# Optimization experiments

Measured on AMD Instinct MI355X. Metric: run time of the kernel, lower is better.

The kernel has to match this reference:

```python
import jax, jax.numpy as jnp
import numpy as np

LN_EPS = 1e-5  # torch.nn.LayerNorm default eps


def setup_inputs() -> dict:
    key = jax.random.key(0)
    k1, k2 = jax.random.split(key)
    x = jax.random.normal(k1, (16384, 2048), dtype=jnp.float32)
    # torch Linear weight layout: [out_features, in_features]
    W = jax.random.normal(k2, (2048, 2048), dtype=jnp.float32) * (1.0 / np.sqrt(2048))
    return {"x": x, "W": W}


def reference(x, W):
    # LayerNorm over last dim, elementwise_affine=False
    mean = jnp.mean(x, axis=-1, keepdims=True)
    var = jnp.mean(jnp.square(x - mean), axis=-1, keepdims=True)
    xn = (x - mean) * jax.lax.rsqrt(var + LN_EPS)
    # Linear (no bias): y = xn @ W.T, then sigmoid
    y = jnp.einsum("td,od->to", xn, W)
    return jax.nn.sigmoid(y)
```

## Files before the change

kernel.cpp:

```cpp
#include <hip/hip_runtime.h>
#include <hip/hip_bf16.h>
#include <stdint.h>


typedef __attribute__((ext_vector_type(4))) float f32x4;
typedef __attribute__((ext_vector_type(8))) __bf16 b16x8;

__device__ __forceinline__ void async16(void* lds, const void* g) {
  __builtin_amdgcn_global_load_lds(
      (const __attribute__((address_space(1))) void*)g,
      (__attribute__((address_space(3))) void*)lds, 16, 0, 0);
}

__device__ __forceinline__ unsigned short f2bf(float f) {
  uint32_t u = __float_as_uint(f);
  u += 0x7FFFu + ((u >> 16) & 1u);
  return (unsigned short)(u >> 16);
}

__global__ __launch_bounds__(256) void ln_bf16_kernel(
    const float* __restrict__ x, unsigned short* __restrict__ xn) {
  const int row = blockIdx.x;
  const int t = threadIdx.x;
  const float4* xr = (const float4*)(x + (size_t)row * 2048);
  float4 a = xr[t];
  float4 b = xr[t + 256];
  float s = a.x + a.y + a.z + a.w + b.x + b.y + b.z + b.w;
  float q = a.x * a.x + a.y * a.y + a.z * a.z + a.w * a.w +
            b.x * b.x + b.y * b.y + b.z * b.z + b.w * b.w;
#pragma unroll
  for (int off = 32; off > 0; off >>= 1) {
    s += __shfl_down(s, off);
    q += __shfl_down(q, off);
  }
  __shared__ float red[8];
  const int w = t >> 6;
  if ((t & 63) == 0) { red[w] = s; red[4 + w] = q; }
  __syncthreads();
  s = red[0] + red[1] + red[2] + red[3];
  q = red[4] + red[5] + red[6] + red[7];
  const float mean = s * (1.0f / 2048.0f);
  const float var = fmaxf(q * (1.0f / 2048.0f) - mean * mean, 0.0f);
  const float scl = rsqrtf(var + 1e-5f);
  ushort4 o0, o1;
  o0.x = f2bf((a.x - mean) * scl);
  o0.y = f2bf((a.y - mean) * scl);
  o0.z = f2bf((a.z - mean) * scl);
  o0.w = f2bf((a.w - mean) * scl);
  o1.x = f2bf((b.x - mean) * scl);
  o1.y = f2bf((b.y - mean) * scl);
  o1.z = f2bf((b.z - mean) * scl);
  o1.w = f2bf((b.w - mean) * scl);
  ushort4* orow = (ushort4*)(xn + (size_t)row * 2048);
  orow[t] = o0;
  orow[t + 256] = o1;
}

__global__ __launch_bounds__(256) void wconv_kernel(
    const float* __restrict__ W, unsigned short* __restrict__ Wb) {
  const size_t i = (size_t)blockIdx.x * 256 + threadIdx.x;
  float4 v = ((const float4*)W)[i];
  ushort4 o;
  o.x = f2bf(v.x);
  o.y = f2bf(v.y);
  o.z = f2bf(v.z);
  o.w = f2bf(v.w);
  ((ushort4*)Wb)[i] = o;
}


#define STG_A(buf, h, kt)                                              \
  do {                                                                 \
    const char* s_ = pA + (size_t)((h) * 128) * 4096 + (kt) * 128;     \
    char* d_ = lds + (buf) * 65536 + (h) * 16384 + tid * 16;           \
    async16(d_, s_);                                                   \
    async16(d_ + 8192, s_ + 64 * 4096);                                \
  } while (0)

#define STG_B(buf, h, kt)                                              \
  do {                                                                 \
    const char* s_ = pB + (size_t)((h) * 128) * 4096 + (kt) * 128;     \
    char* d_ = lds + 32768 + (buf) * 65536 + (h) * 16384 + tid * 16;   \
    async16(d_, s_);                                                   \
    async16(d_ + 8192, s_ + 64 * 4096);                                \
  } while (0)

#define LDA(buf, qm)                                                   \
  do {                                                                 \
    _Pragma("unroll") for (int i_ = 0; i_ < 4; ++i_) {                 \
      const char* p_ = lds + (buf) * 65536 + (qm) * 16384 + abase + i_ * 2048; \
      aF[i_][0] = *(const b16x8*)(p_ + cs0);                           \
      aF[i_][1] = *(const b16x8*)(p_ + cs1);                           \
    }                                                                  \
  } while (0)

#define LDB(dstf, buf, qn)                                             \
  do {                                                                 \
    _Pragma("unroll") for (int j_ = 0; j_ < 2; ++j_) {                 \
      const char* p_ = lds + (buf) * 65536 + (qn) * 16384 + bbase + j_ * 2048; \
      dstf[j_][0] = *(const b16x8*)(p_ + cs0);                         \
      dstf[j_][1] = *(const b16x8*)(p_ + cs1);                         \
    }                                                                  \
  } while (0)

#define MFMA_Q(qm, qn, BF)                                             \
  do {                                                                 \
    __builtin_amdgcn_s_setprio(1);                                     \
    _Pragma("unroll") for (int i_ = 0; i_ < 4; ++i_) {                 \
      _Pragma("unroll") for (int j_ = 0; j_ < 2; ++j_) {               \
        f32x4 c_ = acc[(qm) * 4 + i_][(qn) * 2 + j_];                  \
        c_ = __builtin_amdgcn_mfma_f32_16x16x32_bf16(aF[i_][0], BF[j_][0], c_, 0, 0, 0); \
        c_ = __builtin_amdgcn_mfma_f32_16x16x32_bf16(aF[i_][1], BF[j_][1], c_, 0, 0, 0); \
        acc[(qm) * 4 + i_][(qn) * 2 + j_] = c_;                        \
      }                                                                \
    }                                                                  \
    __builtin_amdgcn_s_setprio(0);                                     \
  } while (0)

#define BAR1                                                           \
  do {                                                                 \
    __builtin_amdgcn_s_barrier();                                      \
    asm volatile("s_waitcnt lgkmcnt(0)" ::: "memory");                 \
    __builtin_amdgcn_sched_barrier(0);                                 \
  } while (0)

#define BAR2                                                           \
  do {                                                                 \
    __builtin_amdgcn_s_barrier();                                      \
    asm volatile("" ::: "memory");                                     \
  } while (0)

#define VMC(n) asm volatile("s_waitcnt vmcnt(" #n ")" ::: "memory")

__global__ __launch_bounds__(512, 2) void gemm8p(
    const unsigned short* __restrict__ A, const unsigned short* __restrict__ B,
    float* __restrict__ C) {
  __shared__ __align__(16) char lds[131072];

  const int bid0 = blockIdx.x;
  const int bid = (bid0 & 7) * 64 + (bid0 >> 3);
  const int bm = bid >> 3;
  const int bn = bid & 7;

  const int tid = threadIdx.x;
  const int w = tid >> 6, l = tid & 63;
  const int wr = w >> 2, wc = w & 3;
  const int fr = l & 15, fg = l >> 4;

  const int arow = tid >> 3;
  const int swz = ((tid & 7) << 4) ^ ((arow & 7) << 4);
  const char* pA = (const char*)A + (size_t)(bm * 256 + arow) * 4096 + swz;
  const char* pB = (const char*)B + (size_t)(bn * 256 + arow) * 4096 + swz;

  const int cswz = (fg << 4) ^ ((fr & 7) << 4);
  const int cs0 = cswz, cs1 = cswz ^ 64;
  const int abase = (wr * 64 + fr) * 128;
  const int bbase = 32768 + (wc * 32 + fr) * 128;

  f32x4 acc[8][4] = {};
  b16x8 aF[4][2], b0F[2][2], b1F[2][2];

  STG_A(0, 0, 0); STG_B(0, 0, 0); STG_B(0, 1, 0); STG_A(0, 1, 0);
  STG_B(1, 0, 1); STG_A(1, 0, 1); STG_B(1, 1, 1);
  VMC(6);
  __builtin_amdgcn_s_barrier();
  asm volatile("" ::: "memory");

#pragma unroll 1
  for (int it = 0; it < 16; ++it) {
    const int t1 = 2 * it + 1, t2 = 2 * it + 2, t3 = 2 * it + 3;
    const bool s2 = (t2 < 32), s3 = (t3 < 32);

    LDA(0, 0); LDB(b0F, 0, 0);
    STG_A(1, 1, t1);
    BAR1; MFMA_Q(0, 0, b0F); BAR2;

    LDB(b1F, 0, 1);
    if (s2) STG_B(0, 0, t2);
    BAR1; MFMA_Q(0, 1, b1F); BAR2;

    LDA(0, 1);
    if (s2) STG_A(0, 0, t2);
    BAR1; MFMA_Q(1, 1, b1F); BAR2;

    if (s2) STG_B(0, 1, t2);
    BAR1; MFMA_Q(1, 0, b0F);
    if (it < 15) { VMC(6); } else { VMC(0); }
    BAR2;

    LDA(1, 0); LDB(b0F, 1, 0);
    if (s2) STG_A(0, 1, t2);
    BAR1; MFMA_Q(0, 0, b0F); BAR2;

    LDB(b1F, 1, 1);
    if (s3) STG_B(1, 0, t3);
    BAR1; MFMA_Q(0, 1, b1F); BAR2;

    LDA(1, 1);
    if (s3) STG_A(1, 0, t3);
    BAR1; MFMA_Q(1, 1, b1F); BAR2;

    if (s3) STG_B(1, 1, t3);
    BAR1; MFMA_Q(1, 0, b0F);
    if (it < 15) { VMC(6); }
    BAR2;
  }

  float* gC = C + (size_t)(bm * 256) * 2048 + bn * 256;
#pragma unroll
  for (int qm = 0; qm < 2; ++qm) {
#pragma unroll
    for (int i = 0; i < 4; ++i) {
#pragma unroll
      for (int qn = 0; qn < 2; ++qn) {
#pragma unroll
        for (int j = 0; j < 2; ++j) {
#pragma unroll
          for (int r = 0; r < 4; ++r) {
            const int row = qm * 128 + wr * 64 + i * 16 + fg * 4 + r;
            const int col = qn * 128 + wc * 32 + j * 16 + fr;
            const float y = acc[qm * 4 + i][qn * 2 + j][r];
            gC[(size_t)row * 2048 + col] = 1.0f / (1.0f + __expf(-y));
          }
        }
      }
    }
  }
}

extern "C" void kernel_launch(void* const* d_in, const int* in_sizes, int n_in,
                              void* d_out, int out_size, void* d_ws, size_t ws_size,
                              hipStream_t stream) {
  const float* x = (const float*)d_in[0];
  const float* W = (const float*)d_in[1];
  float* out = (float*)d_out;

  unsigned short* xnb = (unsigned short*)d_ws;
  unsigned short* Wb =
      (unsigned short*)((char*)d_ws + (size_t)16384 * 2048 * 2);

  ln_bf16_kernel<<<16384, 256, 0, stream>>>(x, xnb);
  wconv_kernel<<<(2048 * 2048 / 4) / 256, 256, 0, stream>>>(W, Wb);
  gemm8p<<<512, 512, 0, stream>>>(xnb, Wb, out);
}
```

Baseline: 169.9 us.

## Switch GEMM to 32x32x16 MFMA, halve barriers, fuse LN and weight conversion

The GEMM inner tiles move from 16x16x32 to 32x32x16 bf16 MFMA, with the LDS fragment loads and the epilogue row mapping rewritten to match. The two barriers per quarter step become one barrier followed by an LDS wait, and the staging order is shuffled. LayerNorm and the fp32-to-bf16 conversion of W now run in one launch that uses extra blocks, saving a kernel launch. The larger MFMA cuts instruction count and fragment loads per FLOP, but dropping the second barrier relies on the remaining ordering to protect buffer reuse.

Result: slower. 180.4 us (+6.2%).

```diff
diff --git a/kernel.cpp b/kernel.cpp
--- a/kernel.cpp
+++ b/kernel.cpp
@@ -4,12 +4,13 @@
 
 
 typedef __attribute__((ext_vector_type(4))) float f32x4;
+typedef __attribute__((ext_vector_type(16))) float f32x16;
 typedef __attribute__((ext_vector_type(8))) __bf16 b16x8;
 
-__device__ __forceinline__ void async16(void* lds, const void* g) {
+__device__ __forceinline__ void async16(void* lds_p, const void* g) {
   __builtin_amdgcn_global_load_lds(
       (const __attribute__((address_space(1))) void*)g,
-      (__attribute__((address_space(3))) void*)lds, 16, 0, 0);
+      (__attribute__((address_space(3))) void*)lds_p, 16, 0, 0);
 }
 
 __device__ __forceinline__ unsigned short f2bf(float f) {
@@ -18,10 +19,19 @@
   return (unsigned short)(u >> 16);
 }
 
-__global__ __launch_bounds__(256) void ln_bf16_kernel(
-    const float* __restrict__ x, unsigned short* __restrict__ xn) {
+__global__ __launch_bounds__(256) void ln_wconv_kernel(
+    const float* __restrict__ x, unsigned short* __restrict__ xn,
+    const float* __restrict__ W, unsigned short* __restrict__ Wb) {
+  const int t = threadIdx.x;
+  if (blockIdx.x >= 16384) {
+    const size_t i = (size_t)(blockIdx.x - 16384) * 256 + t;
+    float4 v = ((const float4*)W)[i];
+    ushort4 o;
+    o.x = f2bf(v.x); o.y = f2bf(v.y); o.z = f2bf(v.z); o.w = f2bf(v.w);
+    ((ushort4*)Wb)[i] = o;
+    return;
+  }
   const int row = blockIdx.x;
-  const int t = threadIdx.x;
   const float4* xr = (const float4*)(x + (size_t)row * 2048);
   float4 a = xr[t];
   float4 b = xr[t + 256];
@@ -56,18 +66,6 @@
   orow[t + 256] = o1;
 }
 
-__global__ __launch_bounds__(256) void wconv_kernel(
-    const float* __restrict__ W, unsigned short* __restrict__ Wb) {
-  const size_t i = (size_t)blockIdx.x * 256 + threadIdx.x;
-  float4 v = ((const float4*)W)[i];
-  ushort4 o;
-  o.x = f2bf(v.x);
-  o.y = f2bf(v.y);
-  o.z = f2bf(v.z);
-  o.w = f2bf(v.w);
-  ((ushort4*)Wb)[i] = o;
-}
-
 
 #define STG_A(buf, h, kt)                                              \
   do {                                                                 \
@@ -87,47 +85,44 @@
 
 #define LDA(buf, qm)                                                   \
   do {                                                                 \
-    _Pragma("unroll") for (int i_ = 0; i_ < 4; ++i_) {                 \
-      const char* p_ = lds + (buf) * 65536 + (qm) * 16384 + abase + i_ * 2048; \
-      aF[i_][0] = *(const b16x8*)(p_ + cs0);                           \
-      aF[i_][1] = *(const b16x8*)(p_ + cs1);                           \
+    const char* base_ = lds + (buf) * 65536 + (qm) * 16384 + rowA;     \
+    _Pragma("unroll") for (int mi_ = 0; mi_ < 2; ++mi_) {              \
+      _Pragma("unroll") for (int s_ = 0; s_ < 4; ++s_) {               \
+        aF[mi_][s_] = *(const b16x8*)(base_ + mi_ * 4096 + ofs[s_]);   \
+      }                                                                \
     }                                                                  \
   } while (0)
 
 #define LDB(dstf, buf, qn)                                             \
   do {                                                                 \
-    _Pragma("unroll") for (int j_ = 0; j_ < 2; ++j_) {                 \
-      const char* p_ = lds + (buf) * 65536 + (qn) * 16384 + bbase + j_ * 2048; \
-      dstf[j_][0] = *(const b16x8*)(p_ + cs0);                         \
-      dstf[j_][1] = *(const b16x8*)(p_ + cs1);                         \
+    const char* base_ = lds + (buf) * 65536 + 32768 + (qn) * 16384 + rowB; \
+    _Pragma("unroll") for (int s_ = 0; s_ < 4; ++s_) {                 \
+      dstf[s_] = *(const b16x8*)(base_ + ofs[s_]);                     \
     }                                                                  \
   } while (0)
 
 #define MFMA_Q(qm, qn, BF)                                             \
   do {                                                                 \
     __builtin_amdgcn_s_setprio(1);                                     \
-    _Pragma("unroll") for (int i_ = 0; i_ < 4; ++i_) {                 \
-      _Pragma("unroll") for (int j_ = 0; j_ < 2; ++j_) {               \
-        f32x4 c_ = acc[(qm) * 4 + i_][(qn) * 2 + j_];                  \
-        c_ = __builtin_amdgcn_mfma_f32_16x16x32_bf16(aF[i_][0], BF[j_][0], c_, 0, 0, 0); \
-        c_ = __builtin_amdgcn_mfma_f32_16x16x32_bf16(aF[i_][1], BF[j_][1], c_, 0, 0, 0); \
-        acc[(qm) * 4 + i_][(qn) * 2 + j_] = c_;                        \
+    _Pragma("unroll") for (int s_ = 0; s_ < 4; ++s_) {                 \
+      _Pragma("unroll") for (int mi_ = 0; mi_ < 2; ++mi_) {            \
+        acc[(qm) * 2 + mi_][qn] = __builtin_amdgcn_mfma_f32_32x32x16_bf16( \
+            aF[mi_][s_], BF[s_], acc[(qm) * 2 + mi_][qn], 0, 0, 0);    \
       }                                                                \
     }                                                                  \
     __builtin_amdgcn_s_setprio(0);                                     \
   } while (0)
 
-#define BAR1                                                           \
+#define BARR                                                           \
   do {                                                                 \
     __builtin_amdgcn_s_barrier();                                      \
+    asm volatile("" ::: "memory");                                     \
+  } while (0)
+
+#define LGKM0                                                          \
+  do {                                                                 \
     asm volatile("s_waitcnt lgkmcnt(0)" ::: "memory");                 \
     __builtin_amdgcn_sched_barrier(0);                                 \
-  } while (0)
-
-#define BAR2                                                           \
-  do {                                                                 \
-    __builtin_amdgcn_s_barrier();                                      \
-    asm volatile("" ::: "memory");                                     \
   } while (0)
 
 #define VMC(n) asm volatile("s_waitcnt vmcnt(" #n ")" ::: "memory")
@@ -145,83 +140,81 @@
   const int tid = threadIdx.x;
   const int w = tid >> 6, l = tid & 63;
   const int wr = w >> 2, wc = w & 3;
-  const int fr = l & 15, fg = l >> 4;
+  const int l31 = l & 31;
+  const int h16 = (l >> 5) * 16;
+  const int sw7 = (l & 7) << 4;
 
   const int arow = tid >> 3;
   const int swz = ((tid & 7) << 4) ^ ((arow & 7) << 4);
   const char* pA = (const char*)A + (size_t)(bm * 256 + arow) * 4096 + swz;
   const char* pB = (const char*)B + (size_t)(bn * 256 + arow) * 4096 + swz;
 
-  const int cswz = (fg << 4) ^ ((fr & 7) << 4);
-  const int cs0 = cswz, cs1 = cswz ^ 64;
-  const int abase = (wr * 64 + fr) * 128;
-  const int bbase = 32768 + (wc * 32 + fr) * 128;
-
-  f32x4 acc[8][4] = {};
-  b16x8 aF[4][2], b0F[2][2], b1F[2][2];
+  int ofs[4];
+#pragma unroll
+  for (int s = 0; s < 4; ++s) ofs[s] = (s * 32 + h16) ^ sw7;
+  const int rowA = (wr * 64 + l31) * 128;
+  const int rowB = (wc * 32 + l31) * 128;
+
+  f32x16 acc[4][2] = {};
+  b16x8 aF[2][4], bF0[4], bF1[4];
 
   STG_A(0, 0, 0); STG_B(0, 0, 0); STG_B(0, 1, 0); STG_A(0, 1, 0);
   STG_B(1, 0, 1); STG_A(1, 0, 1); STG_B(1, 1, 1);
   VMC(6);
-  __builtin_amdgcn_s_barrier();
-  asm volatile("" ::: "memory");
+  BARR;
 
 #pragma unroll 1
   for (int it = 0; it < 16; ++it) {
     const int t1 = 2 * it + 1, t2 = 2 * it + 2, t3 = 2 * it + 3;
-    const bool s2 = (t2 < 32), s3 = (t3 < 32);
-
-    LDA(0, 0); LDB(b0F, 0, 0);
+    const bool s2 = (it < 15);
+
     STG_A(1, 1, t1);
-    BAR1; MFMA_Q(0, 0, b0F); BAR2;
-
-    LDB(b1F, 0, 1);
-    if (s2) STG_B(0, 0, t2);
-    BAR1; MFMA_Q(0, 1, b1F); BAR2;
-
+    LDA(0, 0); LDB(bF0, 0, 0);
+    BARR; LGKM0; MFMA_Q(0, 0, bF0);
+
+    LDB(bF1, 0, 1);
+    BARR; LGKM0; MFMA_Q(0, 1, bF1);
+
+    if (s2) { STG_B(0, 0, t2); STG_A(0, 0, t2); }
     LDA(0, 1);
-    if (s2) STG_A(0, 0, t2);
-    BAR1; MFMA_Q(1, 1, b1F); BAR2;
+    BARR; LGKM0; MFMA_Q(1, 1, bF1);
 
     if (s2) STG_B(0, 1, t2);
-    BAR1; MFMA_Q(1, 0, b0F);
-    if (it < 15) { VMC(6); } else { VMC(0); }
-    BAR2;
-
-    LDA(1, 0); LDB(b0F, 1, 0);
+    BARR; MFMA_Q(1, 0, bF0);
+    if (s2) { VMC(6); } else { VMC(0); }
+
     if (s2) STG_A(0, 1, t2);
-    BAR1; MFMA_Q(0, 0, b0F); BAR2;
-
-    LDB(b1F, 1, 1);
-    if (s3) STG_B(1, 0, t3);
-    BAR1; MFMA_Q(0, 1, b1F); BAR2;
-
+    LDA(1, 0); LDB(bF0, 1, 0);
+    BARR; LGKM0; MFMA_Q(0, 0, bF0);
+
+    LDB(bF1, 1, 1);
+    BARR; LGKM0; MFMA_Q(0, 1, bF1);
+
+    if (s2) { STG_B(1, 0, t3); STG_A(1, 0, t3); }
     LDA(1, 1);
-    if (s3) STG_A(1, 0, t3);
-    BAR1; MFMA_Q(1, 1, b1F); BAR2;
-
-    if (s3) STG_B(1, 1, t3);
-    BAR1; MFMA_Q(1, 0, b0F);
-    if (it < 15) { VMC(6); }
-    BAR2;
+    BARR; LGKM0; MFMA_Q(1, 1, bF1);
+
+    if (s2) STG_B(1, 1, t3);
+    BARR; MFMA_Q(1, 0, bF0);
+    if (s2) VMC(6);
   }
 
   float* gC = C + (size_t)(bm * 256) * 2048 + bn * 256;
+  const int rbase = 4 * (l >> 5);
 #pragma unroll
   for (int qm = 0; qm < 2; ++qm) {
 #pragma unroll
-    for (int i = 0; i < 4; ++i) {
+    for (int mi = 0; mi < 2; ++mi) {
 #pragma unroll
       for (int qn = 0; qn < 2; ++qn) {
-#pragma unroll
-        for (int j = 0; j < 2; ++j) {
-#pragma unroll
-          for (int r = 0; r < 4; ++r) {
-            const int row = qm * 128 + wr * 64 + i * 16 + fg * 4 + r;
-            const int col = qn * 128 + wc * 32 + j * 16 + fr;
-            const float y = acc[qm * 4 + i][qn * 2 + j][r];
-            gC[(size_t)row * 2048 + col] = 1.0f / (1.0f + __expf(-y));
-          }
+        const f32x16 v = acc[qm * 2 + mi][qn];
+        const int col = qn * 128 + wc * 32 + l31;
+        const int row0 = qm * 128 + wr * 64 + mi * 32 + rbase;
+#pragma unroll
+        for (int r = 0; r < 16; ++r) {
+          const int row = row0 + (r & 3) + 8 * (r >> 2);
+          const float y = v[r];
+          gC[(size_t)row * 2048 + col] = 1.0f / (1.0f + __expf(-y));
         }
       }
     }
@@ -239,7 +232,6 @@
   unsigned short* Wb =
       (unsigned short*)((char*)d_ws + (size_t)16384 * 2048 * 2);
 
-  ln_bf16_kernel<<<16384, 256, 0, stream>>>(x, xnb);
-  wconv_kernel<<<(2048 * 2048 / 4) / 256, 256, 0, stream>>>(W, Wb);
+  ln_wconv_kernel<<<16384 + 4096, 256, 0, stream>>>(x, xnb, W, Wb);
   gemm8p<<<512, 512, 0, stream>>>(xnb, Wb, out);
 }
```

## Software-pipeline LDS fragment loads under MFMAs, fuse LN and weight convert

Applied to the files above, without the earlier changes.

Restructures the GEMM main loop so LDS fragment reads for the next quadrant are issued during the current MFMA batch, splitting MFMA and A-fragment loads into K-halves that interleave. This removes the stalls where waves wait on lgkmcnt before each MFMA group. It also merges the LayerNorm and weight bf16-conversion kernels into one launch and uses a hardware reciprocal in the sigmoid epilogue. The reworked barrier/waitcnt placement raises the risk of LDS race hazards and adds register pressure.

Result: faster. 164.6 us (-3.1%).

```diff
diff --git a/kernel.cpp b/kernel.cpp
--- a/kernel.cpp
+++ b/kernel.cpp
@@ -6,10 +6,10 @@
 typedef __attribute__((ext_vector_type(4))) float f32x4;
 typedef __attribute__((ext_vector_type(8))) __bf16 b16x8;
 
-__device__ __forceinline__ void async16(void* lds, const void* g) {
+__device__ __forceinline__ void async16(void* lds_p, const void* g) {
   __builtin_amdgcn_global_load_lds(
       (const __attribute__((address_space(1))) void*)g,
-      (__attribute__((address_space(3))) void*)lds, 16, 0, 0);
+      (__attribute__((address_space(3))) void*)lds_p, 16, 0, 0);
 }
 
 __device__ __forceinline__ unsigned short f2bf(float f) {
@@ -18,10 +18,19 @@
   return (unsigned short)(u >> 16);
 }
 
-__global__ __launch_bounds__(256) void ln_bf16_kernel(
-    const float* __restrict__ x, unsigned short* __restrict__ xn) {
+__global__ __launch_bounds__(256) void ln_wconv_kernel(
+    const float* __restrict__ x, unsigned short* __restrict__ xn,
+    const float* __restrict__ W, unsigned short* __restrict__ Wb) {
+  const int t = threadIdx.x;
+  if (blockIdx.x >= 16384) {
+    const size_t i = (size_t)(blockIdx.x - 16384) * 256 + t;
+    float4 v = ((const float4*)W)[i];
+    ushort4 o;
+    o.x = f2bf(v.x); o.y = f2bf(v.y); o.z = f2bf(v.z); o.w = f2bf(v.w);
+    ((ushort4*)Wb)[i] = o;
+    return;
+  }
   const int row = blockIdx.x;
-  const int t = threadIdx.x;
   const float4* xr = (const float4*)(x + (size_t)row * 2048);
   float4 a = xr[t];
   float4 b = xr[t + 256];
@@ -56,18 +65,6 @@
   orow[t + 256] = o1;
 }
 
-__global__ __launch_bounds__(256) void wconv_kernel(
-    const float* __restrict__ W, unsigned short* __restrict__ Wb) {
-  const size_t i = (size_t)blockIdx.x * 256 + threadIdx.x;
-  float4 v = ((const float4*)W)[i];
-  ushort4 o;
-  o.x = f2bf(v.x);
-  o.y = f2bf(v.y);
-  o.z = f2bf(v.z);
-  o.w = f2bf(v.w);
-  ((ushort4*)Wb)[i] = o;
-}
-
 
 #define STG_A(buf, h, kt)                                              \
   do {                                                                 \
@@ -85,14 +82,15 @@
     async16(d_ + 8192, s_ + 64 * 4096);                                \
   } while (0)
 
-#define LDA(buf, qm)                                                   \
+#define LDA_S(buf, qm, S)                                              \
   do {                                                                 \
     _Pragma("unroll") for (int i_ = 0; i_ < 4; ++i_) {                 \
       const char* p_ = lds + (buf) * 65536 + (qm) * 16384 + abase + i_ * 2048; \
-      aF[i_][0] = *(const b16x8*)(p_ + cs0);                           \
-      aF[i_][1] = *(const b16x8*)(p_ + cs1);                           \
+      aF[i_][S] = *(const b16x8*)(p_ + ((S) ? cs1 : cs0));             \
     }                                                                  \
   } while (0)
+
+#define LDA(buf, qm) do { LDA_S(buf, qm, 0); LDA_S(buf, qm, 1); } while (0)
 
 #define LDB(dstf, buf, qn)                                             \
   do {                                                                 \
@@ -103,33 +101,35 @@
     }                                                                  \
   } while (0)
 
-#define MFMA_Q(qm, qn, BF)                                             \
+#define MFMA_H(qm, qn, BF, S)                                          \
   do {                                                                 \
     __builtin_amdgcn_s_setprio(1);                                     \
     _Pragma("unroll") for (int i_ = 0; i_ < 4; ++i_) {                 \
       _Pragma("unroll") for (int j_ = 0; j_ < 2; ++j_) {               \
-        f32x4 c_ = acc[(qm) * 4 + i_][(qn) * 2 + j_];                  \
-        c_ = __builtin_amdgcn_mfma_f32_16x16x32_bf16(aF[i_][0], BF[j_][0], c_, 0, 0, 0); \
-        c_ = __builtin_amdgcn_mfma_f32_16x16x32_bf16(aF[i_][1], BF[j_][1], c_, 0, 0, 0); \
-        acc[(qm) * 4 + i_][(qn) * 2 + j_] = c_;                        \
+        acc[(qm) * 4 + i_][(qn) * 2 + j_] =                            \
+            __builtin_amdgcn_mfma_f32_16x16x32_bf16(                   \
+                aF[i_][S], BF[j_][S], acc[(qm) * 4 + i_][(qn) * 2 + j_], 0, 0, 0); \
       }                                                                \
     }                                                                  \
     __builtin_amdgcn_s_setprio(0);                                     \
   } while (0)
 
-#define BAR1                                                           \
+#define MFMA_Q(qm, qn, BF)                                             \
+  do { MFMA_H(qm, qn, BF, 0); MFMA_H(qm, qn, BF, 1); } while (0)
+
+#define BARR                                                           \
   do {                                                                 \
     __builtin_amdgcn_s_barrier();                                      \
+    asm volatile("" ::: "memory");                                     \
+  } while (0)
+
+#define LGKM0                                                          \
+  do {                                                                 \
     asm volatile("s_waitcnt lgkmcnt(0)" ::: "memory");                 \
     __builtin_amdgcn_sched_barrier(0);                                 \
   } while (0)
 
-#define BAR2                                                           \
-  do {                                                                 \
-    __builtin_amdgcn_s_barrier();                                      \
-    asm volatile("" ::: "memory");                                     \
-  } while (0)
-
+#define SB0 __builtin_amdgcn_sched_barrier(0)
 #define VMC(n) asm volatile("s_waitcnt vmcnt(" #n ")" ::: "memory")
 
 __global__ __launch_bounds__(512, 2) void gemm8p(
@@ -158,52 +158,69 @@
   const int bbase = 32768 + (wc * 32 + fr) * 128;
 
   f32x4 acc[8][4] = {};
-  b16x8 aF[4][2], b0F[2][2], b1F[2][2];
+  b16x8 aF[4][2], bF0[2][2], bF1[2][2];
 
   STG_A(0, 0, 0); STG_B(0, 0, 0); STG_B(0, 1, 0); STG_A(0, 1, 0);
   STG_B(1, 0, 1); STG_A(1, 0, 1); STG_B(1, 1, 1);
   VMC(6);
-  __builtin_amdgcn_s_barrier();
-  asm volatile("" ::: "memory");
+  BARR;
+  LDA(0, 0); LDB(bF0, 0, 0);
 
 #pragma unroll 1
   for (int it = 0; it < 16; ++it) {
     const int t1 = 2 * it + 1, t2 = 2 * it + 2, t3 = 2 * it + 3;
-    const bool s2 = (t2 < 32), s3 = (t3 < 32);
-
-    LDA(0, 0); LDB(b0F, 0, 0);
+    const bool s2 = (it < 15);
+
     STG_A(1, 1, t1);
-    BAR1; MFMA_Q(0, 0, b0F); BAR2;
-
-    LDB(b1F, 0, 1);
+    BARR; LGKM0;
+    LDB(bF1, 0, 1); SB0;
+    MFMA_Q(0, 0, bF0);
+    BARR;
+
     if (s2) STG_B(0, 0, t2);
-    BAR1; MFMA_Q(0, 1, b1F); BAR2;
-
-    LDA(0, 1);
+    BARR; LGKM0;
+    MFMA_H(0, 1, bF1, 0);
+    SB0; LDA_S(0, 1, 0); SB0;
+    MFMA_H(0, 1, bF1, 1);
+    SB0; LDA_S(0, 1, 1);
+    BARR;
+
     if (s2) STG_A(0, 0, t2);
-    BAR1; MFMA_Q(1, 1, b1F); BAR2;
+    BARR; LGKM0;
+    MFMA_Q(1, 1, bF1);
+    BARR;
 
     if (s2) STG_B(0, 1, t2);
-    BAR1; MFMA_Q(1, 0, b0F);
-    if (it < 15) { VMC(6); } else { VMC(0); }
-    BAR2;
-
-    LDA(1, 0); LDB(b0F, 1, 0);
+    BARR;
+    MFMA_Q(1, 0, bF0);
+    if (s2) { VMC(6); } else { VMC(0); }
+    SB0; LDA(1, 0); LDB(bF0, 1, 0);
+    BARR;
+
     if (s2) STG_A(0, 1, t2);
-    BAR1; MFMA_Q(0, 0, b0F); BAR2;
-
-    LDB(b1F, 1, 1);
-    if (s3) STG_B(1, 0, t3);
-    BAR1; MFMA_Q(0, 1, b1F); BAR2;
-
-    LDA(1, 1);
-    if (s3) STG_A(1, 0, t3);
-    BAR1; MFMA_Q(1, 1, b1F); BAR2;
-
-    if (s3) STG_B(1, 1, t3);
-    BAR1; MFMA_Q(1, 0, b0F);
-    if (it < 15) { VMC(6); }
-    BAR2;
+    BARR; LGKM0;
+    LDB(bF1, 1, 1); SB0;
+    MFMA_Q(0, 0, bF0);
+    BARR;
+
+    if (s2) STG_B(1, 0, t3);
+    BARR; LGKM0;
+    MFMA_H(0, 1, bF1, 0);
+    SB0; LDA_S(1, 1, 0); SB0;
+    MFMA_H(0, 1, bF1, 1);
+    SB0; LDA_S(1, 1, 1);
+    BARR;
+
+    if (s2) STG_A(1, 0, t3);
+    BARR; LGKM0;
+    MFMA_Q(1, 1, bF1);
+    BARR;
+
+    if (s2) STG_B(1, 1, t3);
+    BARR;
+    MFMA_Q(1, 0, bF0);
+    if (s2) { VMC(6); SB0; LDA(0, 0); LDB(bF0, 0, 0); }
+    BARR;
   }
 
   float* gC = C + (size_t)(bm * 256) * 2048 + bn * 256;
@@ -220,7 +237,8 @@
             const int row = qm * 128 + wr * 64 + i * 16 + fg * 4 + r;
             const int col = qn * 128 + wc * 32 + j * 16 + fr;
             const float y = acc[qm * 4 + i][qn * 2 + j][r];
-            gC[(size_t)row * 2048 + col] = 1.0f / (1.0f + __expf(-y));
+            gC[(size_t)row * 2048 + col] =
+                __builtin_amdgcn_rcpf(1.0f + __expf(-y));
           }
         }
       }
@@ -239,7 +257,6 @@
   unsigned short* Wb =
       (unsigned short*)((char*)d_ws + (size_t)16384 * 2048 * 2);
 
-  ln_bf16_kernel<<<16384, 256, 0, stream>>>(x, xnb);
-  wconv_kernel<<<(2048 * 2048 / 4) / 256, 256, 0, stream>>>(W, Wb);
+  ln_wconv_kernel<<<16384 + 4096, 256, 0, stream>>>(x, xnb, W, Wb);
   gemm8p<<<512, 512, 0, stream>>>(xnb, Wb, out);
 }
```
